# Optimization experiments

Measured on AMD Instinct MI355X. Metric: run time of the kernel, lower is better.

Reference implementation:

```python
import jax, jax.numpy as jnp
import numpy as np

N, F, D, R, E = 1024, 256, 64, 11, 2048
ALPHA = 0.2  # LeakyReLU negative slope


def setup_inputs() -> dict:
    key = jax.random.key(0)
    k1, k2, k3, k4, k5, k6 = jax.random.split(key, 6)
    x = jax.random.normal(k1, (N, F), dtype=jnp.float32)
    # Relation-specific weights (ParameterList of [F, D]) stacked: [R, F, D]
    W = jax.random.normal(k2, (R, F, D), dtype=jnp.float32) * (1.414 * (6.0 / (F + D)) ** 0.5)
    # nn.Linear(2*D, 1, bias=False) weight as a vector [2*D]
    a = jax.random.normal(k3, (2 * D,), dtype=jnp.float32) * (1.0 / (2 * D) ** 0.5)
    src_idx = jax.random.randint(k4, (E,), 0, N, dtype=jnp.int32)
    dst_idx = jax.random.randint(k5, (E,), 0, N, dtype=jnp.int32)
    rel_idx = jax.random.randint(k6, (E,), 0, R, dtype=jnp.int32)
    return {"x": x, "W": W, "a": a, "src_idx": src_idx, "dst_idx": dst_idx, "rel_idx": rel_idx}


def reference(x, W, a, src_idx, dst_idx, rel_idx):
    # Per-edge relation weight gather: [E, F, D]
    We = W[rel_idx]
    # einsum('i,ij->ij', emb, W) == row-wise scaling of W by the embedding
    nt = x[dst_idx][:, :, None] * We          # neighbour_temp: [E, F, D]
    ft = x[src_idx][:, :, None] * We          # feature_temp:   [E, F, D]
    hh = jnp.concatenate([ft, nt], axis=-1)   # [E, F, 2D]
    # linear(2D -> 1, no bias) then LeakyReLU: [E, F]
    e = jax.nn.leaky_relu(jnp.einsum('efd,d->ef', hh, a), ALPHA)
    # original: attn = softmax over edge dim (dim=1 of [F, E]); here edges are axis 0
    attn = jax.nn.softmax(e, axis=0)          # [E, F]
    # h[e] = attn[:, e, None] * nt[e]; cat over edges along dim=1 then sum over F
    # => per edge: sum_F attn[e, f] * nt[e, f, :] -> [E, D], flattened to [E*D]
    out = jnp.einsum('ef,efd->ed', attn, nt).reshape(-1)
    return out
```

## Files before the change

kernel.cpp:

```cpp
#include <hip/hip_runtime.h>
#include <hip/hip_bf16.h>

#define NN 1024
#define FF 256
#define DD 64
#define RR 11
#define EE 2048
#define ALPHA 0.2f
#define TPB 512
#define EPT (EE / TPB)

__global__ __launch_bounds__(TPB) void k1_coef(
    const float* __restrict__ x, const float* __restrict__ W,
    const float* __restrict__ a, const int* __restrict__ src,
    const int* __restrict__ dst, const int* __restrict__ rel,
    float* __restrict__ cbuf) {

    const int f    = blockIdx.x;
    const int tid  = threadIdx.x;
    const int wid  = tid >> 6;
    const int lane = tid & 63;

    __shared__ float p_sh[RR], q_sh[RR];
    __shared__ float red_m[8], red_s[8];

    for (int r = wid; r < RR; r += 8) {
        float w  = W[((size_t)r * FF + f) * DD + lane];
        float pa = w * a[lane];
        float qa = w * a[DD + lane];
        #pragma unroll
        for (int o = 32; o > 0; o >>= 1) {
            pa += __shfl_down(pa, o);
            qa += __shfl_down(qa, o);
        }
        if (lane == 0) { p_sh[r] = pa; q_sh[r] = qa; }
    }
    __syncthreads();

    float vals[EPT], xd_v[EPT];
    float m = -INFINITY;
    #pragma unroll
    for (int k = 0; k < EPT; ++k) {
        int e = tid + k * TPB;
        int si = src[e], di = dst[e], r = rel[e];
        float xs = x[(size_t)si * FF + f];
        float xd = x[(size_t)di * FF + f];
        float v = xs * p_sh[r] + xd * q_sh[r];
        v = v > 0.0f ? v : ALPHA * v;
        vals[k] = v;
        xd_v[k] = xd;
        m = fmaxf(m, v);
    }
    #pragma unroll
    for (int o = 32; o > 0; o >>= 1) m = fmaxf(m, __shfl_down(m, o));
    if (lane == 0) red_m[wid] = m;
    __syncthreads();
    m = red_m[0];
    #pragma unroll
    for (int i = 1; i < 8; ++i) m = fmaxf(m, red_m[i]);

    float s = 0.0f;
    #pragma unroll
    for (int k = 0; k < EPT; ++k) {
        vals[k] = expf(vals[k] - m);
        s += vals[k];
    }
    #pragma unroll
    for (int o = 32; o > 0; o >>= 1) s += __shfl_down(s, o);
    if (lane == 0) red_s[wid] = s;
    __syncthreads();
    float st = red_s[0];
    #pragma unroll
    for (int i = 1; i < 8; ++i) st += red_s[i];
    float inv = 1.0f / st;

    #pragma unroll
    for (int k = 0; k < EPT; ++k) {
        int e = tid + k * TPB;
        cbuf[(size_t)e * FF + f] = vals[k] * inv * xd_v[k];
    }
}

__global__ __launch_bounds__(TPB) void k2_out(
    const float* __restrict__ W, const int* __restrict__ rel,
    const float* __restrict__ cbuf, float* __restrict__ out) {

    const int tid  = threadIdx.x;
    const int wid  = tid >> 6;
    const int lane = tid & 63;

    int e  = blockIdx.x * 8 + wid;
    int r  = rel[e];
    const float* __restrict__ Wr = W + (size_t)r * FF * DD;
    const float* __restrict__ ce = cbuf + (size_t)e * FF;
    int fg = lane >> 4;
    int dq = lane & 15;
    float4 acc = make_float4(0.f, 0.f, 0.f, 0.f);
    #pragma unroll 8
    for (int fb = 0; fb < FF; fb += 4) {
        int ff = fb + fg;
        float c = ce[ff];
        float4 w4 = *(const float4*)&Wr[(size_t)ff * DD + dq * 4];
        acc.x = fmaf(c, w4.x, acc.x);
        acc.y = fmaf(c, w4.y, acc.y);
        acc.z = fmaf(c, w4.z, acc.z);
        acc.w = fmaf(c, w4.w, acc.w);
    }
    #pragma unroll
    for (int o = 16; o <= 32; o <<= 1) {
        acc.x += __shfl_xor(acc.x, o);
        acc.y += __shfl_xor(acc.y, o);
        acc.z += __shfl_xor(acc.z, o);
        acc.w += __shfl_xor(acc.w, o);
    }
    if (fg == 0)
        *(float4*)&out[(size_t)e * DD + dq * 4] = acc;
}

extern "C" void kernel_launch(void* const* d_in, const int* in_sizes, int n_in,
                              void* d_out, int out_size, void* d_ws, size_t ws_size,
                              hipStream_t stream) {
    const float* x  = (const float*)d_in[0];
    const float* W  = (const float*)d_in[1];
    const float* a  = (const float*)d_in[2];
    const int* src  = (const int*)d_in[3];
    const int* dst  = (const int*)d_in[4];
    const int* rel  = (const int*)d_in[5];
    float* out      = (float*)d_out;
    float* cbuf     = (float*)d_ws;

    k1_coef<<<FF, TPB, 0, stream>>>(x, W, a, src, dst, rel, cbuf);
    k2_out<<<EE / 8, TPB, 0, stream>>>(W, rel, cbuf, out);
}
```

Measured before the change: 23.63 us.

## Fuse both stages into one persistent kernel with grid barrier and relation-sorted edges

Merges the coefficient and output kernels into a single launch of 256 blocks that synchronise through an atomic counter grid barrier, which removes the second kernel launch and its gap. Block 0 also builds a relation-sorted permutation of edges, padded to groups of 8, so each block's 8 warps share one relation's W slice for better cache reuse. This adds a hipMemsetAsync per call and assumes all 256 blocks are co-resident, and the spin barrier and the serial histogram work in block 0 add latency.

```diff
diff --git a/kernel.cpp b/kernel.cpp
--- a/kernel.cpp
+++ b/kernel.cpp
@@ -7,23 +7,52 @@
 #define RR 11
 #define EE 2048
 #define ALPHA 0.2f
+#define NB 256
 #define TPB 512
 #define EPT (EE / TPB)
+#define PERM_CAP 2176
 
-__global__ __launch_bounds__(TPB) void k1_coef(
+
+__global__ __launch_bounds__(TPB) void gat_fused1(
     const float* __restrict__ x, const float* __restrict__ W,
     const float* __restrict__ a, const int* __restrict__ src,
     const int* __restrict__ dst, const int* __restrict__ rel,
-    float* __restrict__ cbuf) {
+    float* __restrict__ out,
+    int* __restrict__ cnt, int* __restrict__ ntiles_p,
+    int* __restrict__ perm, float* __restrict__ cbuf) {
 
-    const int f    = blockIdx.x;
+    const int b    = blockIdx.x;
     const int tid  = threadIdx.x;
     const int wid  = tid >> 6;
     const int lane = tid & 63;
 
     __shared__ float p_sh[RR], q_sh[RR];
     __shared__ float red_m[8], red_s[8];
+    __shared__ int   hist[16], off_sh[16];
 
+    if (b == 0) {
+        if (tid < 16) hist[tid] = 0;
+        __syncthreads();
+        for (int e = tid; e < EE; e += TPB) atomicAdd(&hist[rel[e]], 1);
+        __syncthreads();
+        if (tid == 0) {
+            int acc = 0;
+            for (int r = 0; r < RR; ++r) {
+                off_sh[r] = acc;
+                acc += (hist[r] + 7) & ~7;
+            }
+            *ntiles_p = acc >> 3;
+        }
+        __syncthreads();
+        for (int i = tid; i < PERM_CAP; i += TPB) perm[i] = -1;
+        __syncthreads();
+        for (int e = tid; e < EE; e += TPB) {
+            int pos = atomicAdd(&off_sh[rel[e]], 1);
+            perm[pos] = e;
+        }
+    }
+
+    const int f = b;
     for (int r = wid; r < RR; r += 8) {
         float w  = W[((size_t)r * FF + f) * DD + lane];
         float pa = w * a[lane];
@@ -79,42 +108,52 @@
         int e = tid + k * TPB;
         cbuf[(size_t)e * FF + f] = vals[k] * inv * xd_v[k];
     }
-}
 
-__global__ __launch_bounds__(TPB) void k2_out(
-    const float* __restrict__ W, const int* __restrict__ rel,
-    const float* __restrict__ cbuf, float* __restrict__ out) {
+    __syncthreads();
+    if (tid == 0) {
+        __hip_atomic_fetch_add(cnt, 1, __ATOMIC_RELEASE,
+                               __HIP_MEMORY_SCOPE_AGENT);
+        while (__hip_atomic_load(cnt, __ATOMIC_RELAXED,
+                                 __HIP_MEMORY_SCOPE_AGENT) < NB) {
+            __builtin_amdgcn_s_sleep(2);
+        }
+        __builtin_amdgcn_fence(__ATOMIC_ACQUIRE, "agent");
+    }
+    __syncthreads();
 
-    const int tid  = threadIdx.x;
-    const int wid  = tid >> 6;
-    const int lane = tid & 63;
-
-    int e  = blockIdx.x * 8 + wid;
-    int r  = rel[e];
-    const float* __restrict__ Wr = W + (size_t)r * FF * DD;
-    const float* __restrict__ ce = cbuf + (size_t)e * FF;
-    int fg = lane >> 4;
-    int dq = lane & 15;
-    float4 acc = make_float4(0.f, 0.f, 0.f, 0.f);
-    #pragma unroll 8
-    for (int fb = 0; fb < FF; fb += 4) {
-        int ff = fb + fg;
-        float c = ce[ff];
-        float4 w4 = *(const float4*)&Wr[(size_t)ff * DD + dq * 4];
-        acc.x = fmaf(c, w4.x, acc.x);
-        acc.y = fmaf(c, w4.y, acc.y);
-        acc.z = fmaf(c, w4.z, acc.z);
-        acc.w = fmaf(c, w4.w, acc.w);
+    {
+        int ntiles = *ntiles_p;
+        for (int t = b; t < ntiles; t += NB) {
+            int e = perm[t * 8 + wid];
+            if (e >= 0) {
+                int r = rel[e];
+                const float* __restrict__ Wr = W + (size_t)r * FF * DD;
+                const float* __restrict__ ce = cbuf + (size_t)e * FF;
+                int fg = lane >> 4;
+                int dq = lane & 15;
+                float4 acc = make_float4(0.f, 0.f, 0.f, 0.f);
+                #pragma unroll 8
+                for (int fb = 0; fb < FF; fb += 4) {
+                    int ff = fb + fg;
+                    float c = ce[ff];
+                    float4 w4 = *(const float4*)&Wr[(size_t)ff * DD + dq * 4];
+                    acc.x = fmaf(c, w4.x, acc.x);
+                    acc.y = fmaf(c, w4.y, acc.y);
+                    acc.z = fmaf(c, w4.z, acc.z);
+                    acc.w = fmaf(c, w4.w, acc.w);
+                }
+                #pragma unroll
+                for (int o = 16; o <= 32; o <<= 1) {
+                    acc.x += __shfl_xor(acc.x, o);
+                    acc.y += __shfl_xor(acc.y, o);
+                    acc.z += __shfl_xor(acc.z, o);
+                    acc.w += __shfl_xor(acc.w, o);
+                }
+                if (fg == 0)
+                    *(float4*)&out[(size_t)e * DD + dq * 4] = acc;
+            }
+        }
     }
-    #pragma unroll
-    for (int o = 16; o <= 32; o <<= 1) {
-        acc.x += __shfl_xor(acc.x, o);
-        acc.y += __shfl_xor(acc.y, o);
-        acc.z += __shfl_xor(acc.z, o);
-        acc.w += __shfl_xor(acc.w, o);
-    }
-    if (fg == 0)
-        *(float4*)&out[(size_t)e * DD + dq * 4] = acc;
 }
 
 extern "C" void kernel_launch(void* const* d_in, const int* in_sizes, int n_in,
@@ -127,8 +166,14 @@
     const int* dst  = (const int*)d_in[4];
     const int* rel  = (const int*)d_in[5];
     float* out      = (float*)d_out;
-    float* cbuf     = (float*)d_ws;
 
-    k1_coef<<<FF, TPB, 0, stream>>>(x, W, a, src, dst, rel, cbuf);
-    k2_out<<<EE / 8, TPB, 0, stream>>>(W, rel, cbuf, out);
+    char* wsb = (char*)d_ws;
+    int*   cnt      = (int*)wsb;
+    int*   ntiles_p = (int*)(wsb + 256);
+    int*   perm     = (int*)(wsb + 512);
+    float* cbuf     = (float*)(wsb + 16384);
+
+    hipMemsetAsync(cnt, 0, 64, stream);
+    gat_fused1<<<NB, TPB, 0, stream>>>(x, W, a, src, dst, rel, out,
+                                       cnt, ntiles_p, perm, cbuf);
 }
```

Result: slower. 54.69 us (+131.4%).

## Recompute attention coefficients in output kernel and group edges by relation

Applied to the files above, without the earlier changes.

The first kernel no longer writes a per-edge per-feature coefficient buffer. It writes only the per-feature softmax max and inverse sum plus the projected p/q values, and block 0 also builds a relation-sorted edge permutation padded to tiles of 8. The second kernel stages p/q and the stats in LDS, recomputes each coefficient from x rows, and processes edges grouped by relation so the blocks in a tile share a W slice in cache. The first kernel also caches the x column in LDS for its gathers. This removes the 2 MB coefficient buffer round trip. In exchange it adds exp work in the second kernel and a serial sort inside block 0 of the first kernel.

```diff
diff --git a/kernel.cpp b/kernel.cpp
--- a/kernel.cpp
+++ b/kernel.cpp
@@ -9,20 +9,29 @@
 #define ALPHA 0.2f
 #define TPB 512
 #define EPT (EE / TPB)
+#define PERM_CAP 2176
+#define PQ_N (FF * RR)
+#define K2_GRID (PERM_CAP / 8)
 
-__global__ __launch_bounds__(TPB) void k1_coef(
+
+__global__ __launch_bounds__(TPB) void k1_stats(
     const float* __restrict__ x, const float* __restrict__ W,
     const float* __restrict__ a, const int* __restrict__ src,
     const int* __restrict__ dst, const int* __restrict__ rel,
-    float* __restrict__ cbuf) {
+    float2* __restrict__ pqT, float2* __restrict__ mxinv,
+    int* __restrict__ perm, int* __restrict__ ntiles_p) {
 
     const int f    = blockIdx.x;
     const int tid  = threadIdx.x;
     const int wid  = tid >> 6;
     const int lane = tid & 63;
 
+    __shared__ float xcol[NN];
     __shared__ float p_sh[RR], q_sh[RR];
     __shared__ float red_m[8], red_s[8];
+    __shared__ int   hist[16], off_sh[16];
+
+    for (int i = tid; i < NN; i += TPB) xcol[i] = x[(size_t)i * FF + f];
 
     for (int r = wid; r < RR; r += 8) {
         float w  = W[((size_t)r * FF + f) * DD + lane];
@@ -36,19 +45,19 @@
         if (lane == 0) { p_sh[r] = pa; q_sh[r] = qa; }
     }
     __syncthreads();
+    if (tid < RR) pqT[f * RR + tid] = make_float2(p_sh[tid], q_sh[tid]);
 
-    float vals[EPT], xd_v[EPT];
+    float vals[EPT];
     float m = -INFINITY;
     #pragma unroll
     for (int k = 0; k < EPT; ++k) {
         int e = tid + k * TPB;
-        int si = src[e], di = dst[e], r = rel[e];
-        float xs = x[(size_t)si * FF + f];
-        float xd = x[(size_t)di * FF + f];
+        float xs = xcol[src[e]];
+        float xd = xcol[dst[e]];
+        int r = rel[e];
         float v = xs * p_sh[r] + xd * q_sh[r];
         v = v > 0.0f ? v : ALPHA * v;
         vals[k] = v;
-        xd_v[k] = xd;
         m = fmaxf(m, v);
     }
     #pragma unroll
@@ -61,10 +70,7 @@
 
     float s = 0.0f;
     #pragma unroll
-    for (int k = 0; k < EPT; ++k) {
-        vals[k] = expf(vals[k] - m);
-        s += vals[k];
-    }
+    for (int k = 0; k < EPT; ++k) s += expf(vals[k] - m);
     #pragma unroll
     for (int o = 32; o > 0; o >>= 1) s += __shfl_down(s, o);
     if (lane == 0) red_s[wid] = s;
@@ -72,34 +78,74 @@
     float st = red_s[0];
     #pragma unroll
     for (int i = 1; i < 8; ++i) st += red_s[i];
-    float inv = 1.0f / st;
 
-    #pragma unroll
-    for (int k = 0; k < EPT; ++k) {
-        int e = tid + k * TPB;
-        cbuf[(size_t)e * FF + f] = vals[k] * inv * xd_v[k];
+    if (tid == 0) mxinv[f] = make_float2(m, 1.0f / st);
+
+    if (f == 0) {
+        if (tid < 16) hist[tid] = 0;
+        __syncthreads();
+        for (int e = tid; e < EE; e += TPB) atomicAdd(&hist[rel[e]], 1);
+        __syncthreads();
+        if (tid == 0) {
+            int acc = 0;
+            for (int r = 0; r < RR; ++r) {
+                off_sh[r] = acc;
+                acc += (hist[r] + 7) & ~7;
+            }
+            *ntiles_p = acc >> 3;
+        }
+        __syncthreads();
+        for (int i = tid; i < PERM_CAP; i += TPB) perm[i] = -1;
+        __syncthreads();
+        for (int e = tid; e < EE; e += TPB) {
+            int pos = atomicAdd(&off_sh[rel[e]], 1);
+            perm[pos] = e;
+        }
     }
 }
 
 __global__ __launch_bounds__(TPB) void k2_out(
-    const float* __restrict__ W, const int* __restrict__ rel,
-    const float* __restrict__ cbuf, float* __restrict__ out) {
+    const float* __restrict__ x, const float* __restrict__ W,
+    const int* __restrict__ src, const int* __restrict__ dst,
+    const int* __restrict__ rel,
+    const float2* __restrict__ pqT, const float2* __restrict__ mxinv,
+    const int* __restrict__ perm, const int* __restrict__ ntiles_p,
+    float* __restrict__ out) {
 
+    const int t    = blockIdx.x;
     const int tid  = threadIdx.x;
     const int wid  = tid >> 6;
     const int lane = tid & 63;
 
-    int e  = blockIdx.x * 8 + wid;
+    if (t >= *ntiles_p) return;
+
+    __shared__ float2 pq_lds[PQ_N];
+    __shared__ float2 mx_lds[FF];
+    for (int i = tid; i < PQ_N; i += TPB) pq_lds[i] = pqT[i];
+    if (tid < FF) mx_lds[tid] = mxinv[tid];
+    __syncthreads();
+
+    int e = perm[t * 8 + wid];
+    if (e < 0) return;
     int r  = rel[e];
-    const float* __restrict__ Wr = W + (size_t)r * FF * DD;
-    const float* __restrict__ ce = cbuf + (size_t)e * FF;
-    int fg = lane >> 4;
-    int dq = lane & 15;
+    int si = src[e], di = dst[e];
+    const float* __restrict__ xrs = x + (size_t)si * FF;
+    const float* __restrict__ xrd = x + (size_t)di * FF;
+    const float* __restrict__ Wr  = W + (size_t)r * FF * DD;
+
+    const int fg = lane >> 4;
+    const int dq = lane & 15;
     float4 acc = make_float4(0.f, 0.f, 0.f, 0.f);
     #pragma unroll 8
     for (int fb = 0; fb < FF; fb += 4) {
         int ff = fb + fg;
-        float c = ce[ff];
+        float xs = xrs[ff];
+        float xd = xrd[ff];
+        float2 pqv = pq_lds[ff * RR + r];
+        float2 mi  = mx_lds[ff];
+        float v = xs * pqv.x + xd * pqv.y;
+        v = v > 0.0f ? v : ALPHA * v;
+        float c = expf(v - mi.x) * mi.y * xd;
         float4 w4 = *(const float4*)&Wr[(size_t)ff * DD + dq * 4];
         acc.x = fmaf(c, w4.x, acc.x);
         acc.y = fmaf(c, w4.y, acc.y);
@@ -127,8 +173,15 @@
     const int* dst  = (const int*)d_in[4];
     const int* rel  = (const int*)d_in[5];
     float* out      = (float*)d_out;
-    float* cbuf     = (float*)d_ws;
 
-    k1_coef<<<FF, TPB, 0, stream>>>(x, W, a, src, dst, rel, cbuf);
-    k2_out<<<EE / 8, TPB, 0, stream>>>(W, rel, cbuf, out);
+    char* wsb = (char*)d_ws;
+    int*    ntiles_p = (int*)wsb;
+    int*    perm     = (int*)(wsb + 256);
+    float2* mxinv    = (float2*)(wsb + 12288);
+    float2* pqT      = (float2*)(wsb + 16384);
+
+    k1_stats<<<FF, TPB, 0, stream>>>(x, W, a, src, dst, rel,
+                                     pqT, mxinv, perm, ntiles_p);
+    k2_out<<<K2_GRID, TPB, 0, stream>>>(x, W, src, dst, rel,
+                                        pqT, mxinv, perm, ntiles_p, out);
 }
```

After: 26.99 us. 14.2% more time.
